# Kernel tuning notes

Hardware: AMD Instinct MI355X
Metric: run time of the kernel (lower is better)

## Reference

```python
import jax, jax.numpy as jnp
import numpy as np

N = 100_000
E = 1_600_000
D = 128
LN_EPS = 1e-5


def _gcn_layer(x, src, dst, W, b, gamma, beta):
    # GCNConv (PyG defaults): linear transform, add self-loops, symmetric norm,
    # scatter-add aggregation, then bias. Followed by LayerNorm + ReLU.
    n = x.shape[0]
    h = x @ W  # [N, out]
    loop = jnp.arange(n, dtype=src.dtype)
    src_f = jnp.concatenate([src, loop])  # [E+N]
    dst_f = jnp.concatenate([dst, loop])
    deg = jax.ops.segment_sum(jnp.ones(src_f.shape[0], dtype=h.dtype), dst_f, num_segments=n)
    dinv = jnp.where(deg > 0, jax.lax.rsqrt(deg), 0.0)
    norm = dinv[src_f] * dinv[dst_f]  # [E+N]
    msg = h[src_f] * norm[:, None]  # [E+N, out] -- dominant HBM traffic
    out = jax.ops.segment_sum(msg, dst_f, num_segments=n) + b
    # LayerNorm over feature dim
    mu = jnp.mean(out, axis=-1, keepdims=True)
    var = jnp.mean(jnp.square(out - mu), axis=-1, keepdims=True)
    ln = (out - mu) * jax.lax.rsqrt(var + LN_EPS) * gamma + beta
    # ReLU; dropout is identity in eval mode
    return jax.nn.relu(ln)


def setup_inputs() -> dict:
    key = jax.random.key(0)
    ks = jax.random.split(key, 10)
    x = jax.random.normal(ks[0], (N, D), dtype=jnp.float32)
    edge_index = jax.random.randint(ks[1], (2, E), 0, N, dtype=jnp.int32)
    s = 1.0 / np.sqrt(D)
    W1 = jax.random.normal(ks[2], (D, D), dtype=jnp.float32) * s
    b1 = jnp.zeros((D,), dtype=jnp.float32)
    g1 = jnp.ones((D,), dtype=jnp.float32)
    be1 = jnp.zeros((D,), dtype=jnp.float32)
    W2 = jax.random.normal(ks[3], (D, D), dtype=jnp.float32) * s
    b2 = jnp.zeros((D,), dtype=jnp.float32)
    g2 = jnp.ones((D,), dtype=jnp.float32)
    be2 = jnp.zeros((D,), dtype=jnp.float32)
    return {"x": x, "edge_index": edge_index, "W1": W1, "b1": b1, "g1": g1,
            "be1": be1, "W2": W2, "b2": b2, "g2": g2, "be2": be2}


def reference(x, edge_index, W1, b1, g1, be1, W2, b2, g2, be2):
    src, dst = edge_index[0], edge_index[1]  # PyG flow: source_to_target
    h = _gcn_layer(x, src, dst, W1, b1, g1, be1)
    h = _gcn_layer(h, src, dst, W2, b2, g2, be2)
    return h
```

## Files before the change

### kernel.cpp

```cpp
#include <hip/hip_runtime.h>

#define D 128
#define NBSHIFT 9
#define NB (1 << NBSHIFT)
#define PEPB 8192
#define BINS 256

typedef __attribute__((ext_vector_type(8))) short bf16x8;
typedef __attribute__((ext_vector_type(4))) float floatx4;

__device__ __forceinline__ float bflo(unsigned int u){ return __uint_as_float(u << 16); }
__device__ __forceinline__ float bfhi(unsigned int u){ return __uint_as_float(u & 0xffff0000u); }
__device__ __forceinline__ unsigned int f2bfbits(float f){
    unsigned int x = __float_as_uint(f);
    return (x + 0x7fffu + ((x >> 16) & 1u)) >> 16;
}

__global__ __launch_bounds__(512) void k_bcount(const int* __restrict__ dst, int* __restrict__ bcnt, int E){
    __shared__ int hist[BINS];
    int t = threadIdx.x;
    int base = blockIdx.x * PEPB;
    if (t < BINS) hist[t] = 0;
    __syncthreads();
#pragma unroll
    for (int j = 0; j < 16; ++j){
        int e = base + j * 512 + t;
        if (e < E) atomicAdd(&hist[dst[e] >> NBSHIFT], 1);
    }
    __syncthreads();
    if (t < BINS && hist[t] > 0) atomicAdd(&bcnt[t], hist[t]);
}

__global__ __launch_bounds__(256) void k_bscan(const int* __restrict__ bcnt, int* __restrict__ bbase,
                                               int* __restrict__ bcur, int* __restrict__ rowStartN, int NBK){
    __shared__ int sc[256];
    int t = threadIdx.x;
    int v = (t < NBK) ? bcnt[t] : 0;
    sc[t] = v;
    __syncthreads();
    for (int off = 1; off < 256; off <<= 1){
        int u = (t >= off) ? sc[t - off] : 0;
        __syncthreads();
        sc[t] += u;
        __syncthreads();
    }
    if (t < NBK){
        int ex = sc[t] - v;
        bbase[t] = ex;
        bcur[t] = ex;
    }
    if (t == 255){
        bbase[NBK] = sc[255];
        *rowStartN = sc[255];
    }
}

__global__ __launch_bounds__(512) void k_bucket(const int* __restrict__ src, const int* __restrict__ dst,
                                                int* __restrict__ bcur, unsigned int* __restrict__ edge1,
                                                int NBK, int E){
    __shared__ int hist[BINS], lstart[BINS], lcur[BINS], gbase[BINS];
    __shared__ unsigned int stage[PEPB];
    int t = threadIdx.x;
    int base = blockIdx.x * PEPB;
    int tot = min(PEPB, E - base);
    if (t < BINS) hist[t] = 0;
    __syncthreads();

    unsigned int ent[16]; int bk[16];
#pragma unroll
    for (int j = 0; j < 16; ++j){
        int e = base + j * 512 + t;
        bool ok = (e < E);
        int s = 0, d = 0;
        if (ok){
            s = src[e]; d = dst[e];
            atomicAdd(&hist[d >> NBSHIFT], 1);
        }
        ent[j] = (unsigned)s | (((unsigned)d & (NB - 1)) << 20);
        bk[j] = ok ? (d >> NBSHIFT) : -1;
    }
    __syncthreads();
    if (t < BINS) lstart[t] = hist[t];
    __syncthreads();
    for (int off = 1; off < BINS; off <<= 1){
        int v = 0;
        if (t < BINS && t >= off) v = lstart[t - off];
        __syncthreads();
        if (t < BINS) lstart[t] += v;
        __syncthreads();
    }
    if (t < BINS){
        int ex = lstart[t] - hist[t];
        lstart[t] = ex;
        lcur[t] = ex;
        if (t < NBK && hist[t] > 0) gbase[t] = atomicAdd(&bcur[t], hist[t]);
    }
    __syncthreads();
#pragma unroll
    for (int j = 0; j < 16; ++j){
        if (bk[j] >= 0){
            int pos = atomicAdd(&lcur[bk[j]], 1);
            stage[pos] = ent[j];
        }
    }
    __syncthreads();
    for (int i = t; i < tot; i += 512){
        unsigned int e1 = stage[i];
        int lo = 0, hi = BINS - 1;
        while (lo < hi){
            int midb = (lo + hi + 1) >> 1;
            if (lstart[midb] <= i) lo = midb; else hi = midb - 1;
        }
        edge1[gbase[lo] + (i - lstart[lo])] = e1;
    }
}

__global__ __launch_bounds__(512) void k_csr2(const unsigned int* __restrict__ edge1,
                                              const int* __restrict__ bbase,
                                              int* __restrict__ rowStart, float* __restrict__ dinv,
                                              int* __restrict__ csr, int N){
    __shared__ int hist[NB];
    __shared__ int sc[NB];
    int b = blockIdx.x, t = threadIdx.x;
    int nbase = b << NBSHIFT;
    int nn = min(N - nbase, NB);
    int ebeg = bbase[b], eend = bbase[b + 1];

    hist[t] = 0;
    __syncthreads();
    for (int i = ebeg + t; i < eend; i += 512)
        atomicAdd(&hist[(edge1[i] >> 20) & (NB - 1)], 1);
    __syncthreads();
    sc[t] = hist[t];
    __syncthreads();
    for (int off = 1; off < NB; off <<= 1){
        int v = (t >= off) ? sc[t - off] : 0;
        __syncthreads();
        sc[t] += v;
        __syncthreads();
    }
    {
        int cur = ebeg + sc[t] - hist[t];
        sc[t] = cur;
        if (t < nn){
            rowStart[nbase + t] = cur;
            dinv[nbase + t] = rsqrtf((float)hist[t] + 1.0f);
        }
    }
    __syncthreads();
    for (int i = ebeg + t; i < eend; i += 512){
        unsigned int p = edge1[i];
        int pos = atomicAdd(&sc[(p >> 20) & (NB - 1)], 1);
        csr[pos] = (int)(p & 0xFFFFFu);
    }
}

__global__ __launch_bounds__(256) void k_wtrans(const float* __restrict__ W1,
                                                const float* __restrict__ W2,
                                                unsigned short* __restrict__ Wt1,
                                                unsigned short* __restrict__ Wt2){
    int i = blockIdx.x * 256 + threadIdx.x;
    const float* Ws; unsigned short* Wd; int j = i;
    if (i < 16384){ Ws = W1; Wd = Wt1; } else { Ws = W2; Wd = Wt2; j -= 16384; }
    int k = j >> 7, n = j & 127;
    Wd[n * 128 + k] = (unsigned short)f2bfbits(Ws[k * 128 + n]);
}

template<bool A_BF16>
__global__ __launch_bounds__(256) void k_gemm(const void* __restrict__ Av,
                                              const unsigned short* __restrict__ Wt,
                                              unsigned short* __restrict__ Hout, int Nrows){
    int wave = threadIdx.x >> 6, lane = threadIdx.x & 63;
    int m = lane & 15, quad = lane >> 4;
    int row0 = blockIdx.x * 64 + wave * 16;
    int arow = row0 + m;
    int arowc = arow < Nrows ? arow : Nrows - 1;

    bf16x8 a[4];
    if (A_BF16){
        const unsigned short* Ap = (const unsigned short*)Av + (size_t)arowc * D + quad * 8;
#pragma unroll
        for (int kt = 0; kt < 4; ++kt) a[kt] = *(const bf16x8*)(Ap + kt * 32);
    } else {
        const float* Ap = (const float*)Av + (size_t)arowc * D + quad * 8;
#pragma unroll
        for (int kt = 0; kt < 4; ++kt){
            float4 v0 = *(const float4*)(Ap + kt * 32);
            float4 v1 = *(const float4*)(Ap + kt * 32 + 4);
            bf16x8 af;
            af[0] = (short)f2bfbits(v0.x); af[1] = (short)f2bfbits(v0.y);
            af[2] = (short)f2bfbits(v0.z); af[3] = (short)f2bfbits(v0.w);
            af[4] = (short)f2bfbits(v1.x); af[5] = (short)f2bfbits(v1.y);
            af[6] = (short)f2bfbits(v1.z); af[7] = (short)f2bfbits(v1.w);
            a[kt] = af;
        }
    }

    floatx4 acc[8];
#pragma unroll
    for (int nt = 0; nt < 8; ++nt) acc[nt] = (floatx4){0.f, 0.f, 0.f, 0.f};

    const unsigned short* Bp = Wt + m * D + quad * 8;
#pragma unroll
    for (int kt = 0; kt < 4; ++kt){
        bf16x8 bk[8];
#pragma unroll
        for (int nt = 0; nt < 8; ++nt) bk[nt] = *(const bf16x8*)(Bp + nt * 16 * D + kt * 32);
#pragma unroll
        for (int nt = 0; nt < 8; ++nt)
            acc[nt] = __builtin_amdgcn_mfma_f32_16x16x32_bf16(a[kt], bk[nt], acc[nt], 0, 0, 0);
    }
#pragma unroll
    for (int nt = 0; nt < 8; ++nt){
#pragma unroll
        for (int r = 0; r < 4; ++r){
            int rr = row0 + quad * 4 + r;
            if (rr < Nrows) Hout[(size_t)rr * D + nt * 16 + m] = (unsigned short)f2bfbits(acc[nt][r]);
        }
    }
}

template<bool OUT_BF16>
__global__ __launch_bounds__(256) void k_agg(const unsigned short* __restrict__ h,
                                             const int* __restrict__ rowStart,
                                             const int* __restrict__ csr,
                                             const float* __restrict__ dinv,
                                             const float* __restrict__ bias,
                                             const float* __restrict__ gamma,
                                             const float* __restrict__ beta,
                                             void* __restrict__ outv, int N){
    int node = blockIdx.x * 4 + (threadIdx.x >> 6);
    if (node >= N) return;
    int lane = threadIdx.x & 63;
    int half = lane >> 5, li = lane & 31;
    const uint2* hv = (const uint2*)h;

    float dv = dinv[node];
    float4 acc = {0.f, 0.f, 0.f, 0.f};
    if (half == 0){
        uint2 hs = hv[(size_t)node * 32 + li];
        float w0 = dv * dv;
        acc.x = bflo(hs.x) * w0; acc.y = bfhi(hs.x) * w0;
        acc.z = bflo(hs.y) * w0; acc.w = bfhi(hs.y) * w0;
    }

    int start = rowStart[node], end = rowStart[node + 1];
    int mid = start + ((end - start + 1) >> 1);
    int i    = half ? mid : start;
    int iend = half ? end : mid;

    for (; i + 4 <= iend; i += 4){
        int s0 = csr[i], s1 = csr[i + 1], s2 = csr[i + 2], s3 = csr[i + 3];
        uint2 h0 = hv[(size_t)s0 * 32 + li];
        uint2 h1 = hv[(size_t)s1 * 32 + li];
        uint2 h2 = hv[(size_t)s2 * 32 + li];
        uint2 h3 = hv[(size_t)s3 * 32 + li];
        float w0 = dinv[s0] * dv, w1 = dinv[s1] * dv, w2 = dinv[s2] * dv, w3 = dinv[s3] * dv;
        acc.x = fmaf(bflo(h0.x), w0, acc.x); acc.y = fmaf(bfhi(h0.x), w0, acc.y);
        acc.z = fmaf(bflo(h0.y), w0, acc.z); acc.w = fmaf(bfhi(h0.y), w0, acc.w);
        acc.x = fmaf(bflo(h1.x), w1, acc.x); acc.y = fmaf(bfhi(h1.x), w1, acc.y);
        acc.z = fmaf(bflo(h1.y), w1, acc.z); acc.w = fmaf(bfhi(h1.y), w1, acc.w);
        acc.x = fmaf(bflo(h2.x), w2, acc.x); acc.y = fmaf(bfhi(h2.x), w2, acc.y);
        acc.z = fmaf(bflo(h2.y), w2, acc.z); acc.w = fmaf(bfhi(h2.y), w2, acc.w);
        acc.x = fmaf(bflo(h3.x), w3, acc.x); acc.y = fmaf(bfhi(h3.x), w3, acc.y);
        acc.z = fmaf(bflo(h3.y), w3, acc.z); acc.w = fmaf(bfhi(h3.y), w3, acc.w);
    }
    for (; i < iend; ++i){
        int s = csr[i];
        float ws = dinv[s] * dv;
        uint2 hs = hv[(size_t)s * 32 + li];
        acc.x = fmaf(bflo(hs.x), ws, acc.x); acc.y = fmaf(bfhi(hs.x), ws, acc.y);
        acc.z = fmaf(bflo(hs.y), ws, acc.z); acc.w = fmaf(bfhi(hs.y), ws, acc.w);
    }

    acc.x += __shfl_xor(acc.x, 32, 64);
    acc.y += __shfl_xor(acc.y, 32, 64);
    acc.z += __shfl_xor(acc.z, 32, 64);
    acc.w += __shfl_xor(acc.w, 32, 64);

    float4 bb = ((const float4*)bias)[li];
    acc.x += bb.x; acc.y += bb.y; acc.z += bb.z; acc.w += bb.w;

    float s1 = acc.x + acc.y + acc.z + acc.w;
    float s2 = acc.x * acc.x + acc.y * acc.y + acc.z * acc.z + acc.w * acc.w;
#pragma unroll
    for (int off = 16; off > 0; off >>= 1){
        s1 += __shfl_xor(s1, off, 64);
        s2 += __shfl_xor(s2, off, 64);
    }
    float mu = s1 * (1.0f / 128.0f);
    float var = s2 * (1.0f / 128.0f) - mu * mu;
    float rstd = rsqrtf(var + 1e-5f);

    float4 gg = ((const float4*)gamma)[li];
    float4 be = ((const float4*)beta)[li];
    float ox = fmaxf(fmaf((acc.x - mu) * rstd, gg.x, be.x), 0.0f);
    float oy = fmaxf(fmaf((acc.y - mu) * rstd, gg.y, be.y), 0.0f);
    float oz = fmaxf(fmaf((acc.z - mu) * rstd, gg.z, be.z), 0.0f);
    float ow = fmaxf(fmaf((acc.w - mu) * rstd, gg.w, be.w), 0.0f);
    if (half == 0){
        if (OUT_BF16){
            uint2 o;
            o.x = f2bfbits(ox) | (f2bfbits(oy) << 16);
            o.y = f2bfbits(oz) | (f2bfbits(ow) << 16);
            ((uint2*)outv)[(size_t)node * 32 + li] = o;
        } else {
            floatx4 o = {ox, oy, oz, ow};
            __builtin_nontemporal_store(o, (floatx4*)outv + (size_t)node * 32 + li);
        }
    }
}

extern "C" void kernel_launch(void* const* d_in, const int* in_sizes, int n_in,
                              void* d_out, int out_size, void* d_ws, size_t ws_size,
                              hipStream_t stream){
    const float* x   = (const float*)d_in[0];
    const int*   ei  = (const int*)d_in[1];
    const float* W1  = (const float*)d_in[2];
    const float* b1  = (const float*)d_in[3];
    const float* g1  = (const float*)d_in[4];
    const float* be1 = (const float*)d_in[5];
    const float* W2  = (const float*)d_in[6];
    const float* b2  = (const float*)d_in[7];
    const float* g2  = (const float*)d_in[8];
    const float* be2 = (const float*)d_in[9];
    float* out = (float*)d_out;

    const int N = in_sizes[0] / D;
    const int E = in_sizes[1] / 2;
    const int* src = ei;
    const int* dst = ei + E;

    char* w = (char*)d_ws;
    size_t off = 0;
    auto alloc = [&](size_t bytes) -> char* {
        char* p = w + off;
        off = (off + bytes + 255) & ~(size_t)255;
        return p;
    };
    const int NBK = (N + NB - 1) >> NBSHIFT;
    int*            bcnt     = (int*)alloc((size_t)BINS * 4);
    int*            bbase    = (int*)alloc((size_t)(NBK + 1) * 4);
    int*            bcur     = (int*)alloc((size_t)BINS * 4);
    int*            rowStart = (int*)alloc((size_t)(N + 1) * 4);
    float*          dinv     = (float*)alloc((size_t)N * 4);
    unsigned int*   edge1    = (unsigned int*)alloc((size_t)E * 4);
    int*            csr      = (int*)alloc((size_t)E * 4);
    unsigned short* wt1      = (unsigned short*)alloc(16384 * 2);
    unsigned short* wt2      = (unsigned short*)alloc(16384 * 2);
    unsigned short* h        = (unsigned short*)alloc((size_t)N * D * 2);
    unsigned short* hmid     = (unsigned short*)d_out;

    (void)hipMemsetAsync(bcnt, 0, (size_t)BINS * 4, stream);

    int gP = (E + PEPB - 1) / PEPB;
    int gG = (N + 63) / 64;
    int gA = (N + 3) / 4;

    k_bcount<<<gP, 512, 0, stream>>>(dst, bcnt, E);
    k_bscan <<<1, 256, 0, stream>>>(bcnt, bbase, bcur, rowStart + N, NBK);
    k_bucket<<<gP, 512, 0, stream>>>(src, dst, bcur, edge1, NBK, E);
    k_csr2  <<<NBK, 512, 0, stream>>>(edge1, bbase, rowStart, dinv, csr, N);
    k_wtrans<<<128, 256, 0, stream>>>(W1, W2, wt1, wt2);

    k_gemm<false><<<gG, 256, 0, stream>>>(x, wt1, h, N);
    k_agg<true>  <<<gA, 256, 0, stream>>>(h, rowStart, csr, dinv, b1, g1, be1, hmid, N);
    k_gemm<true> <<<gG, 256, 0, stream>>>(hmid, wt2, h, N);
    k_agg<false> <<<gA, 256, 0, stream>>>(h, rowStart, csr, dinv, b2, g2, be2, out, N);
}
```

Before: 388.1 us.

## Split aggregation wave into four 16-lane edge groups with 16-byte gathers

The aggregation kernel now splits each node's wavefront into four 16-lane groups, each handling a quarter of the neighbour list and loading 16-byte (8 bf16) rows per lane instead of 8-byte. The first eight neighbour gathers per group are issued unconditionally up front, with out-of-range slots pointing at row 0, to raise memory-level parallelism for average degree around 16. Partial sums are combined with two cross-group shuffles, and the fp32 output store is split across two groups. This costs extra speculative loads of row 0 and more registers per thread, and it pads the csr buffer.

After: 409.6 us. +5.5%, slower.

```diff
diff --git a/kernel.cpp b/kernel.cpp
--- a/kernel.cpp
+++ b/kernel.cpp
@@ -232,81 +232,126 @@
     int node = blockIdx.x * 4 + (threadIdx.x >> 6);
     if (node >= N) return;
     int lane = threadIdx.x & 63;
-    int half = lane >> 5, li = lane & 31;
-    const uint2* hv = (const uint2*)h;
-
+    int q = lane >> 4, li = lane & 15;
+    const uint4* hv4 = (const uint4*)h;
+
+    int start = rowStart[node], end = rowStart[node + 1];
     float dv = dinv[node];
-    float4 acc = {0.f, 0.f, 0.f, 0.f};
-    if (half == 0){
-        uint2 hs = hv[(size_t)node * 32 + li];
-        float w0 = dv * dv;
-        acc.x = bflo(hs.x) * w0; acc.y = bfhi(hs.x) * w0;
-        acc.z = bflo(hs.y) * w0; acc.w = bfhi(hs.y) * w0;
-    }
-
-    int start = rowStart[node], end = rowStart[node + 1];
-    int mid = start + ((end - start + 1) >> 1);
-    int i    = half ? mid : start;
-    int iend = half ? end : mid;
-
-    for (; i + 4 <= iend; i += 4){
-        int s0 = csr[i], s1 = csr[i + 1], s2 = csr[i + 2], s3 = csr[i + 3];
-        uint2 h0 = hv[(size_t)s0 * 32 + li];
-        uint2 h1 = hv[(size_t)s1 * 32 + li];
-        uint2 h2 = hv[(size_t)s2 * 32 + li];
-        uint2 h3 = hv[(size_t)s3 * 32 + li];
-        float w0 = dinv[s0] * dv, w1 = dinv[s1] * dv, w2 = dinv[s2] * dv, w3 = dinv[s3] * dv;
-        acc.x = fmaf(bflo(h0.x), w0, acc.x); acc.y = fmaf(bfhi(h0.x), w0, acc.y);
-        acc.z = fmaf(bflo(h0.y), w0, acc.z); acc.w = fmaf(bfhi(h0.y), w0, acc.w);
-        acc.x = fmaf(bflo(h1.x), w1, acc.x); acc.y = fmaf(bfhi(h1.x), w1, acc.y);
-        acc.z = fmaf(bflo(h1.y), w1, acc.z); acc.w = fmaf(bfhi(h1.y), w1, acc.w);
-        acc.x = fmaf(bflo(h2.x), w2, acc.x); acc.y = fmaf(bfhi(h2.x), w2, acc.y);
-        acc.z = fmaf(bflo(h2.y), w2, acc.z); acc.w = fmaf(bfhi(h2.y), w2, acc.w);
-        acc.x = fmaf(bflo(h3.x), w3, acc.x); acc.y = fmaf(bfhi(h3.x), w3, acc.y);
-        acc.z = fmaf(bflo(h3.y), w3, acc.z); acc.w = fmaf(bfhi(h3.y), w3, acc.w);
-    }
-    for (; i < iend; ++i){
+
+    float a0 = 0.f, a1 = 0.f, a2 = 0.f, a3 = 0.f, a4 = 0.f, a5 = 0.f, a6 = 0.f, a7 = 0.f;
+    if (q == 0){
+        uint4 hs = hv4[(size_t)node * 16 + li];
+        float w = dv * dv;
+        a0 = bflo(hs.x) * w; a1 = bfhi(hs.x) * w;
+        a2 = bflo(hs.y) * w; a3 = bfhi(hs.y) * w;
+        a4 = bflo(hs.z) * w; a5 = bfhi(hs.z) * w;
+        a6 = bflo(hs.w) * w; a7 = bfhi(hs.w) * w;
+    }
+
+    int deg = end - start;
+    int len = (deg + 3) >> 2;
+    int cb = min(start + q * len, end);
+    int ce = min(cb + len, end);
+    int n = ce - cb;
+
+    int s0 = 0, s1 = 0, s2 = 0, s3 = 0, s4 = 0, s5 = 0, s6 = 0, s7 = 0;
+    if (n > 0) s0 = csr[cb + 0];
+    if (n > 1) s1 = csr[cb + 1];
+    if (n > 2) s2 = csr[cb + 2];
+    if (n > 3) s3 = csr[cb + 3];
+    if (n > 4) s4 = csr[cb + 4];
+    if (n > 5) s5 = csr[cb + 5];
+    if (n > 6) s6 = csr[cb + 6];
+    if (n > 7) s7 = csr[cb + 7];
+
+    uint4 h0 = hv4[(size_t)s0 * 16 + li];
+    uint4 h1 = hv4[(size_t)s1 * 16 + li];
+    uint4 h2 = hv4[(size_t)s2 * 16 + li];
+    uint4 h3 = hv4[(size_t)s3 * 16 + li];
+    uint4 h4 = hv4[(size_t)s4 * 16 + li];
+    uint4 h5 = hv4[(size_t)s5 * 16 + li];
+    uint4 h6 = hv4[(size_t)s6 * 16 + li];
+    uint4 h7 = hv4[(size_t)s7 * 16 + li];
+    float w0 = (n > 0) ? dinv[s0] * dv : 0.f;
+    float w1 = (n > 1) ? dinv[s1] * dv : 0.f;
+    float w2 = (n > 2) ? dinv[s2] * dv : 0.f;
+    float w3 = (n > 3) ? dinv[s3] * dv : 0.f;
+    float w4 = (n > 4) ? dinv[s4] * dv : 0.f;
+    float w5 = (n > 5) ? dinv[s5] * dv : 0.f;
+    float w6 = (n > 6) ? dinv[s6] * dv : 0.f;
+    float w7 = (n > 7) ? dinv[s7] * dv : 0.f;
+
+#define FMA8(HH, WW) \
+    a0 = fmaf(bflo(HH.x), WW, a0); a1 = fmaf(bfhi(HH.x), WW, a1); \
+    a2 = fmaf(bflo(HH.y), WW, a2); a3 = fmaf(bfhi(HH.y), WW, a3); \
+    a4 = fmaf(bflo(HH.z), WW, a4); a5 = fmaf(bfhi(HH.z), WW, a5); \
+    a6 = fmaf(bflo(HH.w), WW, a6); a7 = fmaf(bfhi(HH.w), WW, a7);
+    if (n > 0){ FMA8(h0, w0) }
+    if (n > 1){ FMA8(h1, w1) }
+    if (n > 2){ FMA8(h2, w2) }
+    if (n > 3){ FMA8(h3, w3) }
+    if (n > 4){ FMA8(h4, w4) }
+    if (n > 5){ FMA8(h5, w5) }
+    if (n > 6){ FMA8(h6, w6) }
+    if (n > 7){ FMA8(h7, w7) }
+
+    for (int i = cb + 8; i < ce; ++i){
         int s = csr[i];
         float ws = dinv[s] * dv;
-        uint2 hs = hv[(size_t)s * 32 + li];
-        acc.x = fmaf(bflo(hs.x), ws, acc.x); acc.y = fmaf(bfhi(hs.x), ws, acc.y);
-        acc.z = fmaf(bflo(hs.y), ws, acc.z); acc.w = fmaf(bfhi(hs.y), ws, acc.w);
-    }
-
-    acc.x += __shfl_xor(acc.x, 32, 64);
-    acc.y += __shfl_xor(acc.y, 32, 64);
-    acc.z += __shfl_xor(acc.z, 32, 64);
-    acc.w += __shfl_xor(acc.w, 32, 64);
-
-    float4 bb = ((const float4*)bias)[li];
-    acc.x += bb.x; acc.y += bb.y; acc.z += bb.z; acc.w += bb.w;
-
-    float s1 = acc.x + acc.y + acc.z + acc.w;
-    float s2 = acc.x * acc.x + acc.y * acc.y + acc.z * acc.z + acc.w * acc.w;
-#pragma unroll
-    for (int off = 16; off > 0; off >>= 1){
-        s1 += __shfl_xor(s1, off, 64);
-        s2 += __shfl_xor(s2, off, 64);
-    }
-    float mu = s1 * (1.0f / 128.0f);
-    float var = s2 * (1.0f / 128.0f) - mu * mu;
+        uint4 hs = hv4[(size_t)s * 16 + li];
+        FMA8(hs, ws)
+    }
+#undef FMA8
+
+#define RED(A) A += __shfl_xor(A, 16, 64); A += __shfl_xor(A, 32, 64);
+    RED(a0) RED(a1) RED(a2) RED(a3) RED(a4) RED(a5) RED(a6) RED(a7)
+#undef RED
+
+    float4 bb0 = ((const float4*)bias)[li * 2];
+    float4 bb1 = ((const float4*)bias)[li * 2 + 1];
+    a0 += bb0.x; a1 += bb0.y; a2 += bb0.z; a3 += bb0.w;
+    a4 += bb1.x; a5 += bb1.y; a6 += bb1.z; a7 += bb1.w;
+
+    float s1v = a0 + a1 + a2 + a3 + a4 + a5 + a6 + a7;
+    float s2v = a0*a0 + a1*a1 + a2*a2 + a3*a3 + a4*a4 + a5*a5 + a6*a6 + a7*a7;
+#pragma unroll
+    for (int off = 8; off > 0; off >>= 1){
+        s1v += __shfl_xor(s1v, off, 64);
+        s2v += __shfl_xor(s2v, off, 64);
+    }
+    float mu = s1v * (1.0f / 128.0f);
+    float var = s2v * (1.0f / 128.0f) - mu * mu;
     float rstd = rsqrtf(var + 1e-5f);
 
-    float4 gg = ((const float4*)gamma)[li];
-    float4 be = ((const float4*)beta)[li];
-    float ox = fmaxf(fmaf((acc.x - mu) * rstd, gg.x, be.x), 0.0f);
-    float oy = fmaxf(fmaf((acc.y - mu) * rstd, gg.y, be.y), 0.0f);
-    float oz = fmaxf(fmaf((acc.z - mu) * rstd, gg.z, be.z), 0.0f);
-    float ow = fmaxf(fmaf((acc.w - mu) * rstd, gg.w, be.w), 0.0f);
-    if (half == 0){
-        if (OUT_BF16){
-            uint2 o;
-            o.x = f2bfbits(ox) | (f2bfbits(oy) << 16);
-            o.y = f2bfbits(oz) | (f2bfbits(ow) << 16);
-            ((uint2*)outv)[(size_t)node * 32 + li] = o;
-        } else {
-            floatx4 o = {ox, oy, oz, ow};
-            __builtin_nontemporal_store(o, (floatx4*)outv + (size_t)node * 32 + li);
+    float4 gg0 = ((const float4*)gamma)[li * 2];
+    float4 gg1 = ((const float4*)gamma)[li * 2 + 1];
+    float4 be0 = ((const float4*)beta)[li * 2];
+    float4 be1 = ((const float4*)beta)[li * 2 + 1];
+    float o0 = fmaxf(fmaf((a0 - mu) * rstd, gg0.x, be0.x), 0.0f);
+    float o1 = fmaxf(fmaf((a1 - mu) * rstd, gg0.y, be0.y), 0.0f);
+    float o2 = fmaxf(fmaf((a2 - mu) * rstd, gg0.z, be0.z), 0.0f);
+    float o3 = fmaxf(fmaf((a3 - mu) * rstd, gg0.w, be0.w), 0.0f);
+    float o4 = fmaxf(fmaf((a4 - mu) * rstd, gg1.x, be1.x), 0.0f);
+    float o5 = fmaxf(fmaf((a5 - mu) * rstd, gg1.y, be1.y), 0.0f);
+    float o6 = fmaxf(fmaf((a6 - mu) * rstd, gg1.z, be1.z), 0.0f);
+    float o7 = fmaxf(fmaf((a7 - mu) * rstd, gg1.w, be1.w), 0.0f);
+
+    if (OUT_BF16){
+        if (q == 0){
+            uint4 o;
+            o.x = f2bfbits(o0) | (f2bfbits(o1) << 16);
+            o.y = f2bfbits(o2) | (f2bfbits(o3) << 16);
+            o.z = f2bfbits(o4) | (f2bfbits(o5) << 16);
+            o.w = f2bfbits(o6) | (f2bfbits(o7) << 16);
+            ((uint4*)outv)[(size_t)node * 16 + li] = o;
+        }
+    } else {
+        if (q == 0){
+            floatx4 o = {o0, o1, o2, o3};
+            __builtin_nontemporal_store(o, (floatx4*)outv + (size_t)node * 32 + li * 2);
+        } else if (q == 1){
+            floatx4 o = {o4, o5, o6, o7};
+            __builtin_nontemporal_store(o, (floatx4*)outv + (size_t)node * 32 + li * 2 + 1);
         }
     }
 }
@@ -345,7 +390,7 @@
     int*            rowStart = (int*)alloc((size_t)(N + 1) * 4);
     float*          dinv     = (float*)alloc((size_t)N * 4);
     unsigned int*   edge1    = (unsigned int*)alloc((size_t)E * 4);
-    int*            csr      = (int*)alloc((size_t)E * 4);
+    int*            csr      = (int*)alloc((size_t)E * 4 + 64);
     unsigned short* wt1      = (unsigned short*)alloc(16384 * 2);
     unsigned short* wt2      = (unsigned short*)alloc(16384 * 2);
     unsigned short* h        = (unsigned short*)alloc((size_t)N * D * 2);
```

## Split aggregation into feature-group partial kernels with source-side dinv prescaling

Applied to the files above, without the earlier changes.

The GEMM epilogue now multiplies each row by dinv, so aggregation no longer gathers dinv per neighbour. Aggregation is split into four 32-feature groups, interleaved across blocks so each group's gather footprint is smaller and more cache friendly. Each wave processes 4 edges x 16 lanes in parallel, and a padding zero row at index N replaces the tail branch. A separate LayerNorm/ReLU kernel then reads the partial results, which adds an extra bf16 round-trip, one more launch per layer, and an extra rounding step.

Measured after the change: 528.5 us. 36.2% more time.

```diff
diff --git a/kernel.cpp b/kernel.cpp
--- a/kernel.cpp
+++ b/kernel.cpp
@@ -8,6 +8,7 @@
 
 typedef __attribute__((ext_vector_type(8))) short bf16x8;
 typedef __attribute__((ext_vector_type(4))) float floatx4;
+typedef __attribute__((ext_vector_type(2))) float floatx2;
 
 __device__ __forceinline__ float bflo(unsigned int u){ return __uint_as_float(u << 16); }
 __device__ __forceinline__ float bfhi(unsigned int u){ return __uint_as_float(u & 0xffff0000u); }
@@ -169,6 +170,7 @@
 template<bool A_BF16>
 __global__ __launch_bounds__(256) void k_gemm(const void* __restrict__ Av,
                                               const unsigned short* __restrict__ Wt,
+                                              const float* __restrict__ dinv,
                                               unsigned short* __restrict__ Hout, int Nrows){
     int wave = threadIdx.x >> 6, lane = threadIdx.x & 63;
     int m = lane & 15, quad = lane >> 4;
@@ -211,80 +213,77 @@
             acc[nt] = __builtin_amdgcn_mfma_f32_16x16x32_bf16(a[kt], bk[nt], acc[nt], 0, 0, 0);
     }
 #pragma unroll
-    for (int nt = 0; nt < 8; ++nt){
-#pragma unroll
-        for (int r = 0; r < 4; ++r){
-            int rr = row0 + quad * 4 + r;
-            if (rr < Nrows) Hout[(size_t)rr * D + nt * 16 + m] = (unsigned short)f2bfbits(acc[nt][r]);
-        }
+    for (int r = 0; r < 4; ++r){
+        int rr = row0 + quad * 4 + r;
+        if (rr < Nrows){
+            float dvr = dinv[rr];
+#pragma unroll
+            for (int nt = 0; nt < 8; ++nt)
+                Hout[(size_t)rr * D + nt * 16 + m] = (unsigned short)f2bfbits(acc[nt][r] * dvr);
+        }
+    }
+}
+
+__global__ __launch_bounds__(256) void k_aggp(const unsigned int* __restrict__ hp,
+                                              const int* __restrict__ rowStart,
+                                              const int* __restrict__ csr,
+                                              const float* __restrict__ dinv,
+                                              unsigned int* __restrict__ aggP, int N){
+    int bid = blockIdx.x;
+    int xs = bid & 7;
+    int g  = xs >> 1;
+    int chunk = (bid >> 3) * 2 + (xs & 1);
+    int node = chunk * 4 + (threadIdx.x >> 6);
+    if (node >= N) return;
+    int lane = threadIdx.x & 63;
+    int slot = lane >> 4, li = lane & 15;
+    int goff = g * 16 + li;
+
+    int start = rowStart[node], end = rowStart[node + 1];
+    float a0 = 0.f, a1 = 0.f;
+    int i = start - 1;
+    while (i < end){
+        int i0 = i + slot, i1 = i0 + 4, i2 = i0 + 8, i3 = i0 + 12;
+        int s0 = (i0 >= start) ? ((i0 < end) ? csr[i0] : N) : node;
+        int s1 = (i1 < end) ? csr[i1] : N;
+        int s2 = (i2 < end) ? csr[i2] : N;
+        int s3 = (i3 < end) ? csr[i3] : N;
+        unsigned u0 = hp[(size_t)s0 * 64 + goff];
+        unsigned u1 = hp[(size_t)s1 * 64 + goff];
+        unsigned u2 = hp[(size_t)s2 * 64 + goff];
+        unsigned u3 = hp[(size_t)s3 * 64 + goff];
+        a0 += bflo(u0) + bflo(u1) + bflo(u2) + bflo(u3);
+        a1 += bfhi(u0) + bfhi(u1) + bfhi(u2) + bfhi(u3);
+        i += 16;
+    }
+    a0 += __shfl_xor(a0, 16, 64); a0 += __shfl_xor(a0, 32, 64);
+    a1 += __shfl_xor(a1, 16, 64); a1 += __shfl_xor(a1, 32, 64);
+    if (slot == 0){
+        float dv = dinv[node];
+        unsigned o = f2bfbits(a0 * dv) | (f2bfbits(a1 * dv) << 16);
+        aggP[(size_t)g * (size_t)N * 16 + (size_t)node * 16 + li] = o;
     }
 }
 
 template<bool OUT_BF16>
-__global__ __launch_bounds__(256) void k_agg(const unsigned short* __restrict__ h,
-                                             const int* __restrict__ rowStart,
-                                             const int* __restrict__ csr,
-                                             const float* __restrict__ dinv,
-                                             const float* __restrict__ bias,
-                                             const float* __restrict__ gamma,
-                                             const float* __restrict__ beta,
-                                             void* __restrict__ outv, int N){
+__global__ __launch_bounds__(256) void k_lnfin(const unsigned int* __restrict__ aggP,
+                                               const float* __restrict__ bias,
+                                               const float* __restrict__ gamma,
+                                               const float* __restrict__ beta,
+                                               void* __restrict__ outv, int N){
     int node = blockIdx.x * 4 + (threadIdx.x >> 6);
     if (node >= N) return;
     int lane = threadIdx.x & 63;
-    int half = lane >> 5, li = lane & 31;
-    const uint2* hv = (const uint2*)h;
-
-    float dv = dinv[node];
-    float4 acc = {0.f, 0.f, 0.f, 0.f};
-    if (half == 0){
-        uint2 hs = hv[(size_t)node * 32 + li];
-        float w0 = dv * dv;
-        acc.x = bflo(hs.x) * w0; acc.y = bfhi(hs.x) * w0;
-        acc.z = bflo(hs.y) * w0; acc.w = bfhi(hs.y) * w0;
-    }
-
-    int start = rowStart[node], end = rowStart[node + 1];
-    int mid = start + ((end - start + 1) >> 1);
-    int i    = half ? mid : start;
-    int iend = half ? end : mid;
-
-    for (; i + 4 <= iend; i += 4){
-        int s0 = csr[i], s1 = csr[i + 1], s2 = csr[i + 2], s3 = csr[i + 3];
-        uint2 h0 = hv[(size_t)s0 * 32 + li];
-        uint2 h1 = hv[(size_t)s1 * 32 + li];
-        uint2 h2 = hv[(size_t)s2 * 32 + li];
-        uint2 h3 = hv[(size_t)s3 * 32 + li];
-        float w0 = dinv[s0] * dv, w1 = dinv[s1] * dv, w2 = dinv[s2] * dv, w3 = dinv[s3] * dv;
-        acc.x = fmaf(bflo(h0.x), w0, acc.x); acc.y = fmaf(bfhi(h0.x), w0, acc.y);
-        acc.z = fmaf(bflo(h0.y), w0, acc.z); acc.w = fmaf(bfhi(h0.y), w0, acc.w);
-        acc.x = fmaf(bflo(h1.x), w1, acc.x); acc.y = fmaf(bfhi(h1.x), w1, acc.y);
-        acc.z = fmaf(bflo(h1.y), w1, acc.z); acc.w = fmaf(bfhi(h1.y), w1, acc.w);
-        acc.x = fmaf(bflo(h2.x), w2, acc.x); acc.y = fmaf(bfhi(h2.x), w2, acc.y);
-        acc.z = fmaf(bflo(h2.y), w2, acc.z); acc.w = fmaf(bfhi(h2.y), w2, acc.w);
-        acc.x = fmaf(bflo(h3.x), w3, acc.x); acc.y = fmaf(bfhi(h3.x), w3, acc.y);
-        acc.z = fmaf(bflo(h3.y), w3, acc.z); acc.w = fmaf(bfhi(h3.y), w3, acc.w);
-    }
-    for (; i < iend; ++i){
-        int s = csr[i];
-        float ws = dinv[s] * dv;
-        uint2 hs = hv[(size_t)s * 32 + li];
-        acc.x = fmaf(bflo(hs.x), ws, acc.x); acc.y = fmaf(bfhi(hs.x), ws, acc.y);
-        acc.z = fmaf(bflo(hs.y), ws, acc.z); acc.w = fmaf(bfhi(hs.y), ws, acc.w);
-    }
-
-    acc.x += __shfl_xor(acc.x, 32, 64);
-    acc.y += __shfl_xor(acc.y, 32, 64);
-    acc.z += __shfl_xor(acc.z, 32, 64);
-    acc.w += __shfl_xor(acc.w, 32, 64);
-
-    float4 bb = ((const float4*)bias)[li];
-    acc.x += bb.x; acc.y += bb.y; acc.z += bb.z; acc.w += bb.w;
-
-    float s1 = acc.x + acc.y + acc.z + acc.w;
-    float s2 = acc.x * acc.x + acc.y * acc.y + acc.z * acc.z + acc.w * acc.w;
-#pragma unroll
-    for (int off = 16; off > 0; off >>= 1){
+    int g = lane >> 4, li = lane & 15;
+    int p = g * 16 + li;
+    unsigned u = aggP[(size_t)g * (size_t)N * 16 + (size_t)node * 16 + li];
+    float2 bb = ((const float2*)bias)[p];
+    float v0 = bflo(u) + bb.x;
+    float v1 = bfhi(u) + bb.y;
+
+    float s1 = v0 + v1, s2 = v0 * v0 + v1 * v1;
+#pragma unroll
+    for (int off = 1; off < 64; off <<= 1){
         s1 += __shfl_xor(s1, off, 64);
         s2 += __shfl_xor(s2, off, 64);
     }
@@ -292,22 +291,16 @@
     float var = s2 * (1.0f / 128.0f) - mu * mu;
     float rstd = rsqrtf(var + 1e-5f);
 
-    float4 gg = ((const float4*)gamma)[li];
-    float4 be = ((const float4*)beta)[li];
-    float ox = fmaxf(fmaf((acc.x - mu) * rstd, gg.x, be.x), 0.0f);
-    float oy = fmaxf(fmaf((acc.y - mu) * rstd, gg.y, be.y), 0.0f);
-    float oz = fmaxf(fmaf((acc.z - mu) * rstd, gg.z, be.z), 0.0f);
-    float ow = fmaxf(fmaf((acc.w - mu) * rstd, gg.w, be.w), 0.0f);
-    if (half == 0){
-        if (OUT_BF16){
-            uint2 o;
-            o.x = f2bfbits(ox) | (f2bfbits(oy) << 16);
-            o.y = f2bfbits(oz) | (f2bfbits(ow) << 16);
-            ((uint2*)outv)[(size_t)node * 32 + li] = o;
-        } else {
-            floatx4 o = {ox, oy, oz, ow};
-            __builtin_nontemporal_store(o, (floatx4*)outv + (size_t)node * 32 + li);
-        }
+    float2 gg = ((const float2*)gamma)[p];
+    float2 be = ((const float2*)beta)[p];
+    float o0 = fmaxf(fmaf((v0 - mu) * rstd, gg.x, be.x), 0.0f);
+    float o1 = fmaxf(fmaf((v1 - mu) * rstd, gg.y, be.y), 0.0f);
+
+    if (OUT_BF16){
+        ((unsigned*)outv)[(size_t)node * 64 + p] = f2bfbits(o0) | (f2bfbits(o1) << 16);
+    } else {
+        floatx2 o = {o0, o1};
+        __builtin_nontemporal_store(o, (floatx2*)outv + (size_t)node * 64 + p);
     }
 }
 
@@ -345,17 +338,21 @@
     int*            rowStart = (int*)alloc((size_t)(N + 1) * 4);
     float*          dinv     = (float*)alloc((size_t)N * 4);
     unsigned int*   edge1    = (unsigned int*)alloc((size_t)E * 4);
-    int*            csr      = (int*)alloc((size_t)E * 4);
+    int*            csr      = (int*)alloc((size_t)E * 4 + 64);
     unsigned short* wt1      = (unsigned short*)alloc(16384 * 2);
     unsigned short* wt2      = (unsigned short*)alloc(16384 * 2);
-    unsigned short* h        = (unsigned short*)alloc((size_t)N * D * 2);
+    unsigned short* h        = (unsigned short*)alloc((size_t)(N + 1) * D * 2);
+    unsigned int*   aggP     = (unsigned int*)alloc((size_t)4 * N * 16 * 4);
     unsigned short* hmid     = (unsigned short*)d_out;
 
     (void)hipMemsetAsync(bcnt, 0, (size_t)BINS * 4, stream);
+    (void)hipMemsetAsync(h + (size_t)N * D, 0, D * 2, stream);
 
     int gP = (E + PEPB - 1) / PEPB;
     int gG = (N + 63) / 64;
-    int gA = (N + 3) / 4;
+    int chunks = (N + 3) / 4;
+    int gAp = ((chunks + 1) / 2) * 8;
+    int gLn = chunks;
 
     k_bcount<<<gP, 512, 0, stream>>>(dst, bcnt, E);
     k_bscan <<<1, 256, 0, stream>>>(bcnt, bbase, bcur, rowStart + N, NBK);
@@ -363,8 +360,10 @@
     k_csr2  <<<NBK, 512, 0, stream>>>(edge1, bbase, rowStart, dinv, csr, N);
     k_wtrans<<<128, 256, 0, stream>>>(W1, W2, wt1, wt2);
 
-    k_gemm<false><<<gG, 256, 0, stream>>>(x, wt1, h, N);
-    k_agg<true>  <<<gA, 256, 0, stream>>>(h, rowStart, csr, dinv, b1, g1, be1, hmid, N);
-    k_gemm<true> <<<gG, 256, 0, stream>>>(hmid, wt2, h, N);
-    k_agg<false> <<<gA, 256, 0, stream>>>(h, rowStart, csr, dinv, b2, g2, be2, out, N);
-}
+    k_gemm<false><<<gG, 256, 0, stream>>>(x, wt1, dinv, h, N);
+    k_aggp       <<<gAp, 256, 0, stream>>>((const unsigned int*)h, rowStart, csr, dinv, aggP, N);
+    k_lnfin<true><<<gLn, 256, 0, stream>>>(aggP, b1, g1, be1, hmid, N);
+    k_gemm<true> <<<gG, 256, 0, stream>>>(hmid, wt2, dinv, h, N);
+    k_aggp       <<<gAp, 256, 0, stream>>>((const unsigned int*)h, rowStart, csr, dinv, aggP, N);
+    k_lnfin<false><<<gLn, 256, 0, stream>>>(aggP, b2, g2, be2, out, N);
+}
```
